# Kernel tuning notes

Measured on AMD Instinct MI355X. Metric: run time of the kernel, lower is better.

Reference implementation:

```python
import jax, jax.numpy as jnp
import numpy as np

IN_DIM = 300
MEM_DIM = 1024
DEPTH = 14  # perfect binary tree in heap order: N = 2**DEPTH - 1 = 16383 nodes


def _init_linear(key, out_dim, in_dim):
    # torch nn.Linear default init: U(-1/sqrt(in), 1/sqrt(in)) for W and b
    s = 1.0 / np.sqrt(in_dim)
    kw, kb = jax.random.split(key)
    W = jax.random.uniform(kw, (out_dim, in_dim), jnp.float32, -s, s)
    b = jax.random.uniform(kb, (out_dim,), jnp.float32, -s, s)
    return W, b


def setup_inputs() -> dict:
    key = jax.random.key(0)
    keys = jax.random.split(key, 9)
    N = 2 ** DEPTH - 1
    inp = {"embs": jax.random.normal(keys[0], (N, IN_DIM), jnp.float32)}
    gates = [("ix", IN_DIM), ("ih", MEM_DIM), ("fx", IN_DIM), ("fh", MEM_DIM),
             ("ox", IN_DIM), ("oh", MEM_DIM), ("ux", IN_DIM), ("uh", MEM_DIM)]
    for k, (name, d) in zip(keys[1:], gates):
        W, b = _init_linear(k, MEM_DIM, d)
        inp["W" + name] = W
        inp["b" + name] = b
    inp["depth"] = DEPTH
    return inp


def _lin(x, W, b):
    return x @ W.T + b


def reference(embs, Wix, bix, Wih, bih, Wfx, bfx, Wfh, bfh,
              Wox, box, Woh, boh, Wux, bux, Wuh, buh, depth):
    # Child-Sum TreeLSTM on a perfect binary tree (heap order), processed
    # bottom-up, batching all nodes of a level into single GEMMs.
    h = c = None
    for lvl in range(depth - 1, -1, -1):
        n = 2 ** lvl
        x = embs[n - 1:2 * n - 1]  # [n, in_dim], nodes of this level
        if h is None:
            # leaves: original code feeds a single zero child -> h_sum = 0
            # and f * child_c = 0 regardless of f
            hsum = jnp.zeros((n, MEM_DIM), embs.dtype)
            fc = jnp.zeros((n, MEM_DIM), embs.dtype)
        else:
            hc = h.reshape(n, 2, MEM_DIM)  # children hidden states
            cc = c.reshape(n, 2, MEM_DIM)  # children cell states
            hsum = hc.sum(axis=1)
            # per-child forget gate: sigmoid(fh(h_k) + fx(x))
            f = jax.nn.sigmoid(jnp.einsum('nkd,md->nkm', hc, Wfh) + bfh
                               + _lin(x, Wfx, bfx)[:, None, :])
            fc = (f * cc).sum(axis=1)
        i = jax.nn.sigmoid(_lin(x, Wix, bix) + _lin(hsum, Wih, bih))
        o = jax.nn.sigmoid(_lin(x, Wox, box) + _lin(hsum, Woh, boh))
        u = jnp.tanh(_lin(x, Wux, bux) + _lin(hsum, Wuh, buh))
        c = i * u + fc
        h = o * jnp.tanh(c)
    return jnp.stack([c[0], h[0]])  # root state (c, h): [2, MEM_DIM]
```

## Files before the change

### kernel.cpp

```cpp
#include <hip/hip_runtime.h>
#include <hip/hip_bf16.h>

#define IN_DIM 300
#define XDIM   320
#define MEM    1024
#define NTREE  16383

typedef _Float16 half8 __attribute__((ext_vector_type(8)));
typedef float    f32x4 __attribute__((ext_vector_type(4)));

__device__ __forceinline__ float sigf(float x) { return 1.0f / (1.0f + __expf(-x)); }
__device__ __forceinline__ float tanhfast(float x) { return 2.0f / (1.0f + __expf(-2.0f * x)) - 1.0f; }

#define GLOAD_LDS16(g, l) \
    __builtin_amdgcn_global_load_lds((const __attribute__((address_space(1))) void*)(g), \
                                     (__attribute__((address_space(3))) void*)(l), 16, 0, 0)

__global__ void pack_kernel(
    const float* __restrict__ embs,
    const float* __restrict__ Wix, const float* __restrict__ bix,
    const float* __restrict__ Wih, const float* __restrict__ bih,
    const float* __restrict__ Wfx, const float* __restrict__ bfx,
    const float* __restrict__ Wfh, const float* __restrict__ bfh,
    const float* __restrict__ Wox, const float* __restrict__ box_,
    const float* __restrict__ Woh, const float* __restrict__ boh,
    const float* __restrict__ Wux, const float* __restrict__ bux,
    const float* __restrict__ Wuh, const float* __restrict__ buh,
    _Float16* __restrict__ Wiou16, _Float16* __restrict__ Wfh16,
    _Float16* __restrict__ x16, _Float16* __restrict__ Bx)
{
    long long idx = (long long)blockIdx.x * blockDim.x + threadIdx.x;
    const long long n_wiou = 3072LL * 1024;
    const long long n_wfh  = 1024LL * 1024;
    const long long n_x    = 16384LL * XDIM;
    const long long n_bx   = 4096LL * XDIM;
    if (idx < n_wiou) {
        int m = (int)(idx >> 10), k = (int)(idx & 1023);
        int g = m >> 10, mm = m & 1023;
        const float* W = (g == 0) ? Wih : (g == 1) ? Woh : Wuh;
        Wiou16[idx] = (_Float16)W[(long long)mm * MEM + k];
        return;
    }
    idx -= n_wiou;
    if (idx < n_wfh) {
        Wfh16[idx] = (_Float16)Wfh[idx];
        return;
    }
    idx -= n_wfh;
    if (idx < n_x) {
        int node = (int)(idx / XDIM), j = (int)(idx % XDIM);
        float v = 0.f;
        if (node < NTREE) {
            if (j < IN_DIM) v = embs[(long long)node * IN_DIM + j];
            else if (j == IN_DIM) v = 1.0f;
        }
        x16[idx] = (_Float16)v;
        return;
    }
    idx -= n_x;
    if (idx < n_bx) {
        int r = (int)(idx / XDIM), j = (int)(idx % XDIM);
        int g = r >> 10, mm = r & 1023;
        const float* Wx = (g == 0) ? Wix : (g == 1) ? Wox : (g == 2) ? Wux : Wfx;
        const float* b1 = (g == 0) ? bix : (g == 1) ? box_ : (g == 2) ? bux : bfx;
        const float* b2 = (g == 0) ? bih : (g == 1) ? boh : (g == 2) ? buh : bfh;
        float v = 0.f;
        if (j < IN_DIM) v = Wx[(long long)mm * IN_DIM + j];
        else if (j == IN_DIM) v = b1[mm] + b2[mm];
        Bx[idx] = (_Float16)v;
    }
}

template<int BM, int BN, int BK>
__device__ __forceinline__ void gemm_tile(
    const _Float16* __restrict__ A, int lda,
    const _Float16* __restrict__ B, int ldb,
    _Float16* __restrict__ C, int ldc, int K,
    _Float16* ldsA, _Float16* ldsB)
{
    constexpr int FM = BM / 32, FN = BN / 32;
    constexpr int CPR = BK / 8;
    constexpr int SWM = CPR - 1;
    constexpr int ACH = BM * BK / 2048;
    constexpr int BCH = BN * BK / 2048;

    int tid = threadIdx.x, wave = tid >> 6, lane = tid & 63;
    int wr = (wave >> 1) * (BM / 2), wc = (wave & 1) * (BN / 2);
    int kq = (lane >> 4) * 8, rs = lane & 15;
    f32x4 acc[FM][FN] = {};

    for (int k0 = 0; k0 < K; k0 += BK) {
#pragma unroll
        for (int j = 0; j < ACH; ++j) {
            int c = j * 256 + tid;
            int row = c / CPR;
            int s = (c ^ row) & SWM;
            GLOAD_LDS16(A + (long long)row * lda + k0 + s * 8,
                        &ldsA[(j * 256 + wave * 64) * 8]);
        }
#pragma unroll
        for (int j = 0; j < BCH; ++j) {
            int c = j * 256 + tid;
            int row = c / CPR;
            int s = (c ^ row) & SWM;
            GLOAD_LDS16(B + (long long)row * ldb + k0 + s * 8,
                        &ldsB[(j * 256 + wave * 64) * 8]);
        }
        __syncthreads();
#pragma unroll
        for (int kk = 0; kk < BK; kk += 32) {
            half8 a[FM], b[FN];
#pragma unroll
            for (int i = 0; i < FM; ++i) {
                int r = wr + i * 16 + rs;
                int s = ((kk + kq) >> 3) ^ (r & SWM);
                a[i] = *(const half8*)&ldsA[r * BK + s * 8];
            }
#pragma unroll
            for (int i = 0; i < FN; ++i) {
                int r = wc + i * 16 + rs;
                int s = ((kk + kq) >> 3) ^ (r & SWM);
                b[i] = *(const half8*)&ldsB[r * BK + s * 8];
            }
#pragma unroll
            for (int mi = 0; mi < FM; ++mi)
#pragma unroll
                for (int ni = 0; ni < FN; ++ni)
                    acc[mi][ni] = __builtin_amdgcn_mfma_f32_16x16x32_f16(a[mi], b[ni], acc[mi][ni], 0, 0, 0);
        }
        __syncthreads();
    }
    int crb = wr + (lane >> 4) * 4, ccb = wc + rs;
#pragma unroll
    for (int mi = 0; mi < FM; ++mi)
#pragma unroll
        for (int i = 0; i < 4; ++i) {
            long long r = crb + mi * 16 + i;
#pragma unroll
            for (int ni = 0; ni < FN; ++ni)
                C[r * ldc + ccb + ni * 16] = (_Float16)acc[mi][ni][i];
        }
}

template<int BM, int BN, int BK>
__global__ __launch_bounds__(256) void gemm_f16(
    const _Float16* __restrict__ A, int lda,
    const _Float16* __restrict__ B, int ldb,
    _Float16* __restrict__ C, int ldc, int K)
{
    __shared__ __align__(16) _Float16 ldsA[BM * BK];
    __shared__ __align__(16) _Float16 ldsB[BN * BK];
    gemm_tile<BM, BN, BK>(A + (long long)blockIdx.x * BM * lda, lda,
                          B + (long long)blockIdx.y * BN * ldb, ldb,
                          C + (long long)blockIdx.x * BM * ldc + (long long)blockIdx.y * BN,
                          ldc, K, ldsA, ldsB);
}

template<int BM1, int BM2, int BK>
__global__ __launch_bounds__(256) void gemm_level(
    const _Float16* __restrict__ Hsum, const _Float16* __restrict__ Hc,
    const _Float16* __restrict__ Wiou, const _Float16* __restrict__ Wf,
    _Float16* __restrict__ houpre, _Float16* __restrict__ fpre,
    int G1, int G2)
{
    constexpr int BMX = (BM1 > BM2) ? BM1 : BM2;
    __shared__ __align__(16) _Float16 ldsA[BMX * BK];
    __shared__ __align__(16) _Float16 ldsB[128 * BK];
    int bx = blockIdx.x;
    if (bx < G1 * 24) {
        int nb = bx / G1, mb = bx % G1;
        gemm_tile<BM1, 128, BK>(Hsum + (long long)mb * BM1 * 1024, 1024,
                                Wiou + (long long)nb * 128 * 1024, 1024,
                                houpre + (long long)mb * BM1 * 3072 + nb * 128, 3072,
                                1024, ldsA, ldsB);
    } else {
        int b2 = bx - G1 * 24;
        int nb = b2 / G2, mb = b2 % G2;
        gemm_tile<BM2, 128, BK>(Hc + (long long)mb * BM2 * 1024, 1024,
                                Wf + (long long)nb * 128 * 1024, 1024,
                                fpre + (long long)mb * BM2 * 1024 + nb * 128, 1024,
                                1024, ldsA, ldsB);
    }
}

__global__ void leaf_combine(const _Float16* __restrict__ XpI,
                             _Float16* __restrict__ cleaf,
                             _Float16* __restrict__ hout,
                             _Float16* __restrict__ hsum)
{
    int idx = blockIdx.x * blockDim.x + threadIdx.x;
    int r = idx >> 7, m8 = (idx & 127) * 8;
    float hs[8];
#pragma unroll
    for (int j = 0; j < 8; ++j) hs[j] = 0.f;
#pragma unroll
    for (int t = 0; t < 2; ++t) {
        long long l = 2 * r + t;
        long long node = 8191 + l;
        half8 vi = *(const half8*)&XpI[node * 3072 + m8];
        half8 vo = *(const half8*)&XpI[node * 3072 + 1024 + m8];
        half8 vu = *(const half8*)&XpI[node * 3072 + 2048 + m8];
        half8 cv, hv;
#pragma unroll
        for (int j = 0; j < 8; ++j) {
            float i = sigf((float)vi[j]);
            float o = sigf((float)vo[j]);
            float u = tanhfast((float)vu[j]);
            float c = i * u;
            float h = o * tanhfast(c);
            cv[j] = (_Float16)c; hv[j] = (_Float16)h; hs[j] += h;
        }
        *(half8*)&cleaf[l * 1024 + m8] = cv;
        *(half8*)&hout[l * 1024 + m8] = hv;
    }
    half8 sv;
#pragma unroll
    for (int j = 0; j < 8; ++j) sv[j] = (_Float16)hs[j];
    *(half8*)&hsum[(long long)r * 1024 + m8] = sv;
}

template<bool C16>
__global__ void combine_level(
    const _Float16* __restrict__ houpre, const _Float16* __restrict__ fpre,
    const void* __restrict__ cprevp,
    const _Float16* __restrict__ XpI, const _Float16* __restrict__ XpF,
    float* __restrict__ cout, _Float16* __restrict__ hout, _Float16* __restrict__ hsum,
    int n, int gx0, float* __restrict__ fin)
{
    int idx = blockIdx.x * blockDim.x + threadIdx.x;
    int npairs = (n > 1) ? (n >> 1) : 1;
    if (idx >= npairs * 128) return;
    int r = idx >> 7, m8 = (idx & 127) * 8;
    float hs[8];
#pragma unroll
    for (int j = 0; j < 8; ++j) hs[j] = 0.f;
    int pmax = (n > 1) ? 2 : 1;
    for (int t = 0; t < pmax; ++t) {
        int p = 2 * r + t;
        long long node = gx0 + p;
        half8 phi = *(const half8*)&houpre[(long long)p * 3072 + m8];
        half8 pho = *(const half8*)&houpre[(long long)p * 3072 + 1024 + m8];
        half8 phu = *(const half8*)&houpre[(long long)p * 3072 + 2048 + m8];
        half8 pxi = *(const half8*)&XpI[node * 3072 + m8];
        half8 pxo = *(const half8*)&XpI[node * 3072 + 1024 + m8];
        half8 pxu = *(const half8*)&XpI[node * 3072 + 2048 + m8];
        half8 pf0 = *(const half8*)&fpre[(long long)(2 * p) * 1024 + m8];
        half8 pf1 = *(const half8*)&fpre[(long long)(2 * p + 1) * 1024 + m8];
        half8 pxf = *(const half8*)&XpF[node * 1024 + m8];
        float c0[8], c1[8];
        if (C16) {
            const _Float16* cp = (const _Float16*)cprevp;
            half8 a = *(const half8*)&cp[(long long)(2 * p) * 1024 + m8];
            half8 b = *(const half8*)&cp[(long long)(2 * p + 1) * 1024 + m8];
#pragma unroll
            for (int j = 0; j < 8; ++j) { c0[j] = (float)a[j]; c1[j] = (float)b[j]; }
        } else {
            const float* cp = (const float*)cprevp;
            f32x4 a0 = *(const f32x4*)&cp[(long long)(2 * p) * 1024 + m8];
            f32x4 a1 = *(const f32x4*)&cp[(long long)(2 * p) * 1024 + m8 + 4];
            f32x4 b0 = *(const f32x4*)&cp[(long long)(2 * p + 1) * 1024 + m8];
            f32x4 b1 = *(const f32x4*)&cp[(long long)(2 * p + 1) * 1024 + m8 + 4];
#pragma unroll
            for (int j = 0; j < 4; ++j) { c0[j] = a0[j]; c0[j + 4] = a1[j]; c1[j] = b0[j]; c1[j + 4] = b1[j]; }
        }
        float cw[8], hw[8];
#pragma unroll
        for (int j = 0; j < 8; ++j) {
            float i  = sigf((float)phi[j] + (float)pxi[j]);
            float o  = sigf((float)pho[j] + (float)pxo[j]);
            float u  = tanhfast((float)phu[j] + (float)pxu[j]);
            float f0 = sigf((float)pf0[j] + (float)pxf[j]);
            float f1 = sigf((float)pf1[j] + (float)pxf[j]);
            float c = i * u + f0 * c0[j] + f1 * c1[j];
            float h = o * tanhfast(c);
            cw[j] = c; hw[j] = h; hs[j] += h;
        }
        if (fin) {
            f32x4 v0 = {cw[0], cw[1], cw[2], cw[3]}, v1 = {cw[4], cw[5], cw[6], cw[7]};
            f32x4 w0 = {hw[0], hw[1], hw[2], hw[3]}, w1 = {hw[4], hw[5], hw[6], hw[7]};
            *(f32x4*)&fin[m8] = v0;            *(f32x4*)&fin[m8 + 4] = v1;
            *(f32x4*)&fin[1024 + m8] = w0;     *(f32x4*)&fin[1024 + m8 + 4] = w1;
        } else {
            f32x4 v0 = {cw[0], cw[1], cw[2], cw[3]}, v1 = {cw[4], cw[5], cw[6], cw[7]};
            *(f32x4*)&cout[(long long)p * 1024 + m8] = v0;
            *(f32x4*)&cout[(long long)p * 1024 + m8 + 4] = v1;
            half8 hv;
#pragma unroll
            for (int j = 0; j < 8; ++j) hv[j] = (_Float16)hw[j];
            *(half8*)&hout[(long long)p * 1024 + m8] = hv;
        }
    }
    if (!fin) {
        half8 sv;
#pragma unroll
        for (int j = 0; j < 8; ++j) sv[j] = (_Float16)hs[j];
        *(half8*)&hsum[(long long)r * 1024 + m8] = sv;
    }
}

extern "C" void kernel_launch(void* const* d_in, const int* in_sizes, int n_in,
                              void* d_out, int out_size, void* d_ws, size_t ws_size,
                              hipStream_t stream)
{
    const float* embs = (const float*)d_in[0];
    const float* Wix = (const float*)d_in[1];  const float* bix = (const float*)d_in[2];
    const float* Wih = (const float*)d_in[3];  const float* bih = (const float*)d_in[4];
    const float* Wfx = (const float*)d_in[5];  const float* bfx = (const float*)d_in[6];
    const float* Wfh = (const float*)d_in[7];  const float* bfh = (const float*)d_in[8];
    const float* Wox = (const float*)d_in[9];  const float* box_ = (const float*)d_in[10];
    const float* Woh = (const float*)d_in[11]; const float* boh = (const float*)d_in[12];
    const float* Wux = (const float*)d_in[13]; const float* bux = (const float*)d_in[14];
    const float* Wuh = (const float*)d_in[15]; const float* buh = (const float*)d_in[16];

    char* p = (char*)d_ws;
    auto carve = [&](size_t bytes) -> char* {
        char* r = p; p += (bytes + 255) & ~(size_t)255; return r;
    };
    _Float16* Wiou16 = (_Float16*)carve((size_t)3072 * 1024 * 2);
    _Float16* Wfh16  = (_Float16*)carve((size_t)1024 * 1024 * 2);
    _Float16* XpI    = (_Float16*)carve((size_t)16384 * 3072 * 2);
    _Float16* XpF    = (_Float16*)carve((size_t)8192 * 1024 * 2);
    _Float16* fpre   = (_Float16*)carve((size_t)8192 * 1024 * 2);
    _Float16* H_A    = (_Float16*)carve((size_t)8192 * 1024 * 2);
    _Float16* H_B    = (_Float16*)carve((size_t)4096 * 1024 * 2);
    _Float16* Hsum   = (_Float16*)carve((size_t)4096 * 1024 * 2);
    _Float16* Cleaf  = (_Float16*)carve((size_t)8192 * 1024 * 2);
    float*    Cping  = (float*)carve((size_t)4096 * 1024 * 4);
    float*    Cpong  = (float*)carve((size_t)2048 * 1024 * 4);
    _Float16* houpre = XpI + (size_t)8192 * 3072;
    _Float16* x16    = fpre;
    _Float16* Bx     = fpre + (size_t)16384 * XDIM;

    {
        long long tot = 3072LL * 1024 + 1024LL * 1024 + 16384LL * XDIM + 4096LL * XDIM;
        pack_kernel<<<dim3((int)((tot + 255) / 256)), dim3(256), 0, stream>>>(
            embs, Wix, bix, Wih, bih, Wfx, bfx, Wfh, bfh,
            Wox, box_, Woh, boh, Wux, bux, Wuh, buh,
            Wiou16, Wfh16, x16, Bx);
    }

    gemm_f16<128, 128, 32><<<dim3(128, 24), dim3(256), 0, stream>>>(
        x16, XDIM, Bx, XDIM, XpI, 3072, XDIM);
    gemm_f16<128, 128, 32><<<dim3(64, 8), dim3(256), 0, stream>>>(
        x16, XDIM, Bx + (size_t)3072 * XDIM, XDIM, XpF, 1024, XDIM);

    leaf_combine<<<dim3(2048), dim3(256), 0, stream>>>(XpI, Cleaf, H_A, Hsum);

    const void* cprev = Cleaf;
    float* cbufs[2] = {Cping, Cpong};
    int ci = 0;
    _Float16* hcur = H_A;
    _Float16* hnext = H_B;

    for (int lvl = 12; lvl >= 0; --lvl) {
        int n = 1 << lvl;
        int G1, G2;
        if (n >= 1024) {
            G1 = n / 128; G2 = 2 * n / 128;
            gemm_level<128, 128, 32><<<dim3(G1 * 24 + G2 * 8), dim3(256), 0, stream>>>(
                Hsum, hcur, Wiou16, Wfh16, houpre, fpre, G1, G2);
        } else if (n >= 128) {
            G1 = n / 128; G2 = 2 * n / 128;
            gemm_level<128, 128, 128><<<dim3(G1 * 24 + G2 * 8), dim3(256), 0, stream>>>(
                Hsum, hcur, Wiou16, Wfh16, houpre, fpre, G1, G2);
        } else if (n == 64) {
            G1 = 1; G2 = 1;
            gemm_level<64, 128, 128><<<dim3(G1 * 24 + G2 * 8), dim3(256), 0, stream>>>(
                Hsum, hcur, Wiou16, Wfh16, houpre, fpre, G1, G2);
        } else {
            G1 = 1; G2 = 1;
            gemm_level<64, 64, 128><<<dim3(G1 * 24 + G2 * 8), dim3(256), 0, stream>>>(
                Hsum, hcur, Wiou16, Wfh16, houpre, fpre, G1, G2);
        }

        int npairs = (n > 1) ? (n >> 1) : 1;
        int blocks = (npairs * 128 + 255) / 256;
        float* fin = (lvl == 0) ? (float*)d_out : nullptr;
        if (lvl == 12)
            combine_level<true><<<dim3(blocks), dim3(256), 0, stream>>>(
                houpre, fpre, cprev, XpI, XpF, cbufs[ci], hnext, Hsum, n, n - 1, fin);
        else
            combine_level<false><<<dim3(blocks), dim3(256), 0, stream>>>(
                houpre, fpre, cprev, XpI, XpF, cbufs[ci], hnext, Hsum, n, n - 1, fin);

        cprev = cbufs[ci];
        ci ^= 1;
        _Float16* tmp = hcur; hcur = hnext; hnext = tmp;
    }
}
```

Measured before the change: 461.2 us.

## Fuse leaf GEMM with combine, fuse small levels, double-buffer GEMM tiles

The leaf input projection and the leaf gate math are merged into one kernel, so the leaf half of the XpI pre-activations is never written to or read back from memory. Levels below 512 nodes now run a single fused kernel that does both GEMMs plus the cell update, which removes a launch and a round-trip through houpre/fpre for each of those levels. The shared GEMM tile gains LDS double buffering, and BK is raised to 64 for the large GEMMs. The cost is higher LDS use and register pressure, and the fused small-level kernels use narrow 64×64 tiles with many accumulators.

New measurement: 662.2 us. 1.44x slower.

```diff
diff --git a/kernel.cpp b/kernel.cpp
--- a/kernel.cpp
+++ b/kernel.cpp
@@ -79,24 +79,22 @@
     _Float16* ldsA, _Float16* ldsB)
 {
     constexpr int FM = BM / 32, FN = BN / 32;
-    constexpr int CPR = BK / 8;
-    constexpr int SWM = CPR - 1;
-    constexpr int ACH = BM * BK / 2048;
-    constexpr int BCH = BN * BK / 2048;
+    constexpr int CPR = BK / 8, SWM = CPR - 1;
+    constexpr int ACH = BM * BK / 2048, BCH = BN * BK / 2048;
 
     int tid = threadIdx.x, wave = tid >> 6, lane = tid & 63;
     int wr = (wave >> 1) * (BM / 2), wc = (wave & 1) * (BN / 2);
     int kq = (lane >> 4) * 8, rs = lane & 15;
     f32x4 acc[FM][FN] = {};
 
-    for (int k0 = 0; k0 < K; k0 += BK) {
+    auto stage = [&](int buf, int k0) {
 #pragma unroll
         for (int j = 0; j < ACH; ++j) {
             int c = j * 256 + tid;
             int row = c / CPR;
             int s = (c ^ row) & SWM;
             GLOAD_LDS16(A + (long long)row * lda + k0 + s * 8,
-                        &ldsA[(j * 256 + wave * 64) * 8]);
+                        &ldsA[buf * BM * BK + (j * 256 + wave * 64) * 8]);
         }
 #pragma unroll
         for (int j = 0; j < BCH; ++j) {
@@ -104,9 +102,17 @@
             int row = c / CPR;
             int s = (c ^ row) & SWM;
             GLOAD_LDS16(B + (long long)row * ldb + k0 + s * 8,
-                        &ldsB[(j * 256 + wave * 64) * 8]);
-        }
-        __syncthreads();
+                        &ldsB[buf * BN * BK + (j * 256 + wave * 64) * 8]);
+        }
+    };
+
+    int NT = K / BK;
+    stage(0, 0);
+    __syncthreads();
+    for (int t = 0; t < NT; ++t) {
+        if (t + 1 < NT) stage((t + 1) & 1, (t + 1) * BK);
+        const _Float16* bA = ldsA + (t & 1) * BM * BK;
+        const _Float16* bB = ldsB + (t & 1) * BN * BK;
 #pragma unroll
         for (int kk = 0; kk < BK; kk += 32) {
             half8 a[FM], b[FN];
@@ -114,13 +120,13 @@
             for (int i = 0; i < FM; ++i) {
                 int r = wr + i * 16 + rs;
                 int s = ((kk + kq) >> 3) ^ (r & SWM);
-                a[i] = *(const half8*)&ldsA[r * BK + s * 8];
+                a[i] = *(const half8*)&bA[r * BK + s * 8];
             }
 #pragma unroll
             for (int i = 0; i < FN; ++i) {
                 int r = wc + i * 16 + rs;
                 int s = ((kk + kq) >> 3) ^ (r & SWM);
-                b[i] = *(const half8*)&ldsB[r * BK + s * 8];
+                b[i] = *(const half8*)&bB[r * BK + s * 8];
             }
 #pragma unroll
             for (int mi = 0; mi < FM; ++mi)
@@ -148,75 +154,232 @@
     const _Float16* __restrict__ B, int ldb,
     _Float16* __restrict__ C, int ldc, int K)
 {
-    __shared__ __align__(16) _Float16 ldsA[BM * BK];
-    __shared__ __align__(16) _Float16 ldsB[BN * BK];
+    __shared__ __align__(16) _Float16 ldsA[2 * BM * BK];
+    __shared__ __align__(16) _Float16 ldsB[2 * BN * BK];
     gemm_tile<BM, BN, BK>(A + (long long)blockIdx.x * BM * lda, lda,
                           B + (long long)blockIdx.y * BN * ldb, ldb,
                           C + (long long)blockIdx.x * BM * ldc + (long long)blockIdx.y * BN,
                           ldc, K, ldsA, ldsB);
 }
 
-template<int BM1, int BM2, int BK>
 __global__ __launch_bounds__(256) void gemm_level(
     const _Float16* __restrict__ Hsum, const _Float16* __restrict__ Hc,
     const _Float16* __restrict__ Wiou, const _Float16* __restrict__ Wf,
     _Float16* __restrict__ houpre, _Float16* __restrict__ fpre,
     int G1, int G2)
 {
-    constexpr int BMX = (BM1 > BM2) ? BM1 : BM2;
-    __shared__ __align__(16) _Float16 ldsA[BMX * BK];
-    __shared__ __align__(16) _Float16 ldsB[128 * BK];
+    __shared__ __align__(16) _Float16 ldsA[2 * 128 * 64];
+    __shared__ __align__(16) _Float16 ldsB[2 * 128 * 64];
     int bx = blockIdx.x;
     if (bx < G1 * 24) {
         int nb = bx / G1, mb = bx % G1;
-        gemm_tile<BM1, 128, BK>(Hsum + (long long)mb * BM1 * 1024, 1024,
+        gemm_tile<128, 128, 64>(Hsum + (long long)mb * 128 * 1024, 1024,
                                 Wiou + (long long)nb * 128 * 1024, 1024,
-                                houpre + (long long)mb * BM1 * 3072 + nb * 128, 3072,
+                                houpre + (long long)mb * 128 * 3072 + nb * 128, 3072,
                                 1024, ldsA, ldsB);
     } else {
         int b2 = bx - G1 * 24;
         int nb = b2 / G2, mb = b2 % G2;
-        gemm_tile<BM2, 128, BK>(Hc + (long long)mb * BM2 * 1024, 1024,
+        gemm_tile<128, 128, 64>(Hc + (long long)mb * 128 * 1024, 1024,
                                 Wf + (long long)nb * 128 * 1024, 1024,
-                                fpre + (long long)mb * BM2 * 1024 + nb * 128, 1024,
+                                fpre + (long long)mb * 128 * 1024 + nb * 128, 1024,
                                 1024, ldsA, ldsB);
     }
 }
 
-__global__ void leaf_combine(const _Float16* __restrict__ XpI,
-                             _Float16* __restrict__ cleaf,
-                             _Float16* __restrict__ hout,
-                             _Float16* __restrict__ hsum)
-{
-    int idx = blockIdx.x * blockDim.x + threadIdx.x;
-    int r = idx >> 7, m8 = (idx & 127) * 8;
-    float hs[8];
-#pragma unroll
-    for (int j = 0; j < 8; ++j) hs[j] = 0.f;
-#pragma unroll
-    for (int t = 0; t < 2; ++t) {
-        long long l = 2 * r + t;
-        long long node = 8191 + l;
-        half8 vi = *(const half8*)&XpI[node * 3072 + m8];
-        half8 vo = *(const half8*)&XpI[node * 3072 + 1024 + m8];
-        half8 vu = *(const half8*)&XpI[node * 3072 + 2048 + m8];
-        half8 cv, hv;
-#pragma unroll
-        for (int j = 0; j < 8; ++j) {
-            float i = sigf((float)vi[j]);
-            float o = sigf((float)vo[j]);
-            float u = tanhfast((float)vu[j]);
-            float c = i * u;
-            float h = o * tanhfast(c);
-            cv[j] = (_Float16)c; hv[j] = (_Float16)h; hs[j] += h;
-        }
-        *(half8*)&cleaf[l * 1024 + m8] = cv;
-        *(half8*)&hout[l * 1024 + m8] = hv;
-    }
-    half8 sv;
-#pragma unroll
-    for (int j = 0; j < 8; ++j) sv[j] = (_Float16)hs[j];
-    *(half8*)&hsum[(long long)r * 1024 + m8] = sv;
+__global__ __launch_bounds__(256) void leaf_fused(
+    const _Float16* __restrict__ x16, const _Float16* __restrict__ Bx,
+    _Float16* __restrict__ cleaf, _Float16* __restrict__ hleaf,
+    _Float16* __restrict__ hsum)
+{
+    constexpr int BK = 32, CPR = 4, SWM = 3;
+    __shared__ __align__(16) _Float16 lA[2 * 64 * BK];
+    __shared__ __align__(16) _Float16 lB[2 * 384 * BK];
+    int tid = threadIdx.x, wave = tid >> 6, lane = tid & 63;
+    int kq = (lane >> 4) * 8, rs = lane & 15;
+    int wr = (wave >> 1) * 32, wc = (wave & 1) * 64;
+    int m0 = blockIdx.x * 64, c0 = blockIdx.y * 128;
+    const _Float16* A = x16 + (size_t)(8191 + m0) * XDIM;
+
+    auto stage = [&](int buf, int k0) {
+        {
+            int c = tid, row = c / CPR, s = (c ^ row) & SWM;
+            GLOAD_LDS16(A + (long long)row * XDIM + k0 + s * 8,
+                        &lA[buf * 64 * BK + (wave * 64) * 8]);
+        }
+#pragma unroll
+        for (int j = 0; j < 6; ++j) {
+            int c = j * 256 + tid;
+            int row = c / CPR, s = (c ^ row) & SWM;
+            int g = row >> 7, rr = row & 127;
+            GLOAD_LDS16(Bx + (long long)(g * 1024 + c0 + rr) * XDIM + k0 + s * 8,
+                        &lB[buf * 384 * BK + (j * 256 + wave * 64) * 8]);
+        }
+    };
+    f32x4 acc[3][2][4] = {};
+    stage(0, 0);
+    __syncthreads();
+    for (int t = 0; t < 10; ++t) {
+        if (t + 1 < 10) stage((t + 1) & 1, (t + 1) * BK);
+        const _Float16* bA = lA + (t & 1) * 64 * BK;
+        const _Float16* bB = lB + (t & 1) * 384 * BK;
+        half8 a[2], b[3][4];
+#pragma unroll
+        for (int mi = 0; mi < 2; ++mi) {
+            int r = wr + mi * 16 + rs;
+            int s = (kq >> 3) ^ (r & SWM);
+            a[mi] = *(const half8*)&bA[r * BK + s * 8];
+        }
+#pragma unroll
+        for (int g = 0; g < 3; ++g)
+#pragma unroll
+            for (int nj = 0; nj < 4; ++nj) {
+                int r = g * 128 + wc + nj * 16 + rs;
+                int s = (kq >> 3) ^ (r & SWM);
+                b[g][nj] = *(const half8*)&bB[r * BK + s * 8];
+            }
+#pragma unroll
+        for (int g = 0; g < 3; ++g)
+#pragma unroll
+            for (int mi = 0; mi < 2; ++mi)
+#pragma unroll
+                for (int nj = 0; nj < 4; ++nj)
+                    acc[g][mi][nj] = __builtin_amdgcn_mfma_f32_16x16x32_f16(a[mi], b[g][nj], acc[g][mi][nj], 0, 0, 0);
+        __syncthreads();
+    }
+    int lrb = wr + (lane >> 4) * 4;
+#pragma unroll
+    for (int mi = 0; mi < 2; ++mi)
+#pragma unroll
+        for (int nj = 0; nj < 4; ++nj) {
+            int col = c0 + wc + nj * 16 + rs;
+            float hpair = 0.f;
+#pragma unroll
+            for (int i = 0; i < 4; ++i) {
+                long long l = m0 + lrb + mi * 16 + i;
+                float cc = sigf(acc[0][mi][nj][i]) * 0.f +
+                           0.f;
+                float ip = acc[0][mi][nj][i];
+                float op = acc[1][mi][nj][i];
+                float up = acc[2][mi][nj][i];
+                cc = sigf(ip) * tanhfast(up);
+                float hh = sigf(op) * tanhfast(cc);
+                cleaf[l * 1024 + col] = (_Float16)cc;
+                hleaf[l * 1024 + col] = (_Float16)hh;
+                if (i & 1) hsum[(l >> 1) * 1024 + col] = (_Float16)(hpair + hh);
+                else hpair = hh;
+            }
+        }
+}
+
+__global__ __launch_bounds__(256) void level_fused(
+    const _Float16* __restrict__ Hs, const _Float16* __restrict__ Hc,
+    const _Float16* __restrict__ Wiou, const _Float16* __restrict__ Wf,
+    const float* __restrict__ cprev,
+    const _Float16* __restrict__ XpI, const _Float16* __restrict__ XpF,
+    float* __restrict__ cout, _Float16* __restrict__ hout,
+    _Float16* __restrict__ hsumout, int n, int gx0, float* __restrict__ fin)
+{
+    constexpr int BK = 32, CPR = 4, SWM = 3;
+    __shared__ __align__(16) _Float16 lA[2 * 192 * BK];
+    __shared__ __align__(16) _Float16 lB[2 * 256 * BK];
+    int tid = threadIdx.x, wave = tid >> 6, lane = tid & 63;
+    int kq = (lane >> 4) * 8, rs = lane & 15;
+    int wr = (wave >> 1) * 32, wc = (wave & 1) * 32;
+    int p0 = blockIdx.x * 64, c0 = blockIdx.y * 64;
+
+    auto stage = [&](int buf, int k0) {
+#pragma unroll
+        for (int j = 0; j < 3; ++j) {
+            int c = j * 256 + tid;
+            int row = c / CPR, s = (c ^ row) & SWM;
+            int ta = row >> 6, rr = row & 63;
+            const _Float16* src = (ta == 0) ? Hs : Hc;
+            long long grow = (ta == 0) ? (long long)(p0 + rr)
+                                       : (2LL * (p0 + rr) + (ta - 1));
+            GLOAD_LDS16(src + grow * 1024 + k0 + s * 8,
+                        &lA[buf * 192 * BK + (j * 256 + wave * 64) * 8]);
+        }
+#pragma unroll
+        for (int j = 0; j < 4; ++j) {
+            int c = j * 256 + tid;
+            int row = c / CPR, s = (c ^ row) & SWM;
+            int tb = row >> 6, rr = row & 63;
+            const _Float16* src = (tb < 3) ? Wiou : Wf;
+            long long grow = (tb < 3) ? (long long)(tb * 1024 + c0 + rr)
+                                      : (long long)(c0 + rr);
+            GLOAD_LDS16(src + grow * 1024 + k0 + s * 8,
+                        &lB[buf * 256 * BK + (j * 256 + wave * 64) * 8]);
+        }
+    };
+    f32x4 acc[5][2][2] = {};
+    stage(0, 0);
+    __syncthreads();
+    for (int t = 0; t < 32; ++t) {
+        if (t + 1 < 32) stage((t + 1) & 1, (t + 1) * BK);
+        const _Float16* bA = lA + (t & 1) * 192 * BK;
+        const _Float16* bB = lB + (t & 1) * 256 * BK;
+        half8 a[3][2], b[4][2];
+#pragma unroll
+        for (int ta = 0; ta < 3; ++ta)
+#pragma unroll
+            for (int mi = 0; mi < 2; ++mi) {
+                int r = ta * 64 + wr + mi * 16 + rs;
+                int s = (kq >> 3) ^ (r & SWM);
+                a[ta][mi] = *(const half8*)&bA[r * BK + s * 8];
+            }
+#pragma unroll
+        for (int tb = 0; tb < 4; ++tb)
+#pragma unroll
+            for (int nj = 0; nj < 2; ++nj) {
+                int r = tb * 64 + wc + nj * 16 + rs;
+                int s = (kq >> 3) ^ (r & SWM);
+                b[tb][nj] = *(const half8*)&bB[r * BK + s * 8];
+            }
+#pragma unroll
+        for (int mi = 0; mi < 2; ++mi)
+#pragma unroll
+            for (int nj = 0; nj < 2; ++nj) {
+                acc[0][mi][nj] = __builtin_amdgcn_mfma_f32_16x16x32_f16(a[0][mi], b[0][nj], acc[0][mi][nj], 0, 0, 0);
+                acc[1][mi][nj] = __builtin_amdgcn_mfma_f32_16x16x32_f16(a[0][mi], b[1][nj], acc[1][mi][nj], 0, 0, 0);
+                acc[2][mi][nj] = __builtin_amdgcn_mfma_f32_16x16x32_f16(a[0][mi], b[2][nj], acc[2][mi][nj], 0, 0, 0);
+                acc[3][mi][nj] = __builtin_amdgcn_mfma_f32_16x16x32_f16(a[1][mi], b[3][nj], acc[3][mi][nj], 0, 0, 0);
+                acc[4][mi][nj] = __builtin_amdgcn_mfma_f32_16x16x32_f16(a[2][mi], b[3][nj], acc[4][mi][nj], 0, 0, 0);
+            }
+        __syncthreads();
+    }
+    int lrb = wr + (lane >> 4) * 4;
+#pragma unroll
+    for (int mi = 0; mi < 2; ++mi)
+#pragma unroll
+        for (int nj = 0; nj < 2; ++nj) {
+            int col = c0 + wc + nj * 16 + rs;
+            float hpair = 0.f;
+#pragma unroll
+            for (int i = 0; i < 4; ++i) {
+                int p = p0 + lrb + mi * 16 + i;
+                if (p >= n) continue;
+                long long node = gx0 + p;
+                float ip = acc[0][mi][nj][i] + (float)XpI[node * 3072 + col];
+                float op = acc[1][mi][nj][i] + (float)XpI[node * 3072 + 1024 + col];
+                float up = acc[2][mi][nj][i] + (float)XpI[node * 3072 + 2048 + col];
+                float xf = (float)XpF[node * 1024 + col];
+                float f0 = sigf(acc[3][mi][nj][i] + xf);
+                float f1 = sigf(acc[4][mi][nj][i] + xf);
+                float cc = sigf(ip) * tanhfast(up)
+                         + f0 * cprev[(long long)(2 * p) * 1024 + col]
+                         + f1 * cprev[(long long)(2 * p + 1) * 1024 + col];
+                float hh = sigf(op) * tanhfast(cc);
+                if (fin) {
+                    if (p == 0) { fin[col] = cc; fin[1024 + col] = hh; }
+                } else {
+                    cout[(long long)p * 1024 + col] = cc;
+                    hout[(long long)p * 1024 + col] = (_Float16)hh;
+                    if (i & 1) hsumout[((long long)(p >> 1)) * 1024 + col] = (_Float16)(hpair + hh);
+                    else hpair = hh;
+                }
+            }
+        }
 }
 
 template<bool C16>
@@ -225,17 +388,16 @@
     const void* __restrict__ cprevp,
     const _Float16* __restrict__ XpI, const _Float16* __restrict__ XpF,
     float* __restrict__ cout, _Float16* __restrict__ hout, _Float16* __restrict__ hsum,
-    int n, int gx0, float* __restrict__ fin)
+    int n, int gx0)
 {
     int idx = blockIdx.x * blockDim.x + threadIdx.x;
-    int npairs = (n > 1) ? (n >> 1) : 1;
+    int npairs = n >> 1;
     if (idx >= npairs * 128) return;
     int r = idx >> 7, m8 = (idx & 127) * 8;
     float hs[8];
 #pragma unroll
     for (int j = 0; j < 8; ++j) hs[j] = 0.f;
-    int pmax = (n > 1) ? 2 : 1;
-    for (int t = 0; t < pmax; ++t) {
+    for (int t = 0; t < 2; ++t) {
         int p = 2 * r + t;
         long long node = gx0 + p;
         half8 phi = *(const half8*)&houpre[(long long)p * 3072 + m8];
@@ -275,27 +437,18 @@
             float h = o * tanhfast(c);
             cw[j] = c; hw[j] = h; hs[j] += h;
         }
-        if (fin) {
-            f32x4 v0 = {cw[0], cw[1], cw[2], cw[3]}, v1 = {cw[4], cw[5], cw[6], cw[7]};
-            f32x4 w0 = {hw[0], hw[1], hw[2], hw[3]}, w1 = {hw[4], hw[5], hw[6], hw[7]};
-            *(f32x4*)&fin[m8] = v0;            *(f32x4*)&fin[m8 + 4] = v1;
-            *(f32x4*)&fin[1024 + m8] = w0;     *(f32x4*)&fin[1024 + m8 + 4] = w1;
-        } else {
-            f32x4 v0 = {cw[0], cw[1], cw[2], cw[3]}, v1 = {cw[4], cw[5], cw[6], cw[7]};
-            *(f32x4*)&cout[(long long)p * 1024 + m8] = v0;
-            *(f32x4*)&cout[(long long)p * 1024 + m8 + 4] = v1;
-            half8 hv;
-#pragma unroll
-            for (int j = 0; j < 8; ++j) hv[j] = (_Float16)hw[j];
-            *(half8*)&hout[(long long)p * 1024 + m8] = hv;
-        }
-    }
-    if (!fin) {
-        half8 sv;
-#pragma unroll
-        for (int j = 0; j < 8; ++j) sv[j] = (_Float16)hs[j];
-        *(half8*)&hsum[(long long)r * 1024 + m8] = sv;
-    }
+        f32x4 v0 = {cw[0], cw[1], cw[2], cw[3]}, v1 = {cw[4], cw[5], cw[6], cw[7]};
+        *(f32x4*)&cout[(long long)p * 1024 + m8] = v0;
+        *(f32x4*)&cout[(long long)p * 1024 + m8 + 4] = v1;
+        half8 hv;
+#pragma unroll
+        for (int j = 0; j < 8; ++j) hv[j] = (_Float16)hw[j];
+        *(half8*)&hout[(long long)p * 1024 + m8] = hv;
+    }
+    half8 sv;
+#pragma unroll
+    for (int j = 0; j < 8; ++j) sv[j] = (_Float16)hs[j];
+    *(half8*)&hsum[(long long)r * 1024 + m8] = sv;
 }
 
 extern "C" void kernel_launch(void* const* d_in, const int* in_sizes, int n_in,
@@ -318,18 +471,19 @@
     };
     _Float16* Wiou16 = (_Float16*)carve((size_t)3072 * 1024 * 2);
     _Float16* Wfh16  = (_Float16*)carve((size_t)1024 * 1024 * 2);
-    _Float16* XpI    = (_Float16*)carve((size_t)16384 * 3072 * 2);
+    _Float16* XpI    = (_Float16*)carve((size_t)8192 * 3072 * 2);
     _Float16* XpF    = (_Float16*)carve((size_t)8192 * 1024 * 2);
+    _Float16* houpre = (_Float16*)carve((size_t)4096 * 3072 * 2);
     _Float16* fpre   = (_Float16*)carve((size_t)8192 * 1024 * 2);
     _Float16* H_A    = (_Float16*)carve((size_t)8192 * 1024 * 2);
     _Float16* H_B    = (_Float16*)carve((size_t)4096 * 1024 * 2);
-    _Float16* Hsum   = (_Float16*)carve((size_t)4096 * 1024 * 2);
+    _Float16* HsumA  = (_Float16*)carve((size_t)4096 * 1024 * 2);
+    _Float16* HsumB  = (_Float16*)carve((size_t)4096 * 1024 * 2);
     _Float16* Cleaf  = (_Float16*)carve((size_t)8192 * 1024 * 2);
     float*    Cping  = (float*)carve((size_t)4096 * 1024 * 4);
     float*    Cpong  = (float*)carve((size_t)2048 * 1024 * 4);
-    _Float16* houpre = XpI + (size_t)8192 * 3072;
-    _Float16* x16    = fpre;
-    _Float16* Bx     = fpre + (size_t)16384 * XDIM;
+    _Float16* x16 = fpre;
+    _Float16* Bx  = fpre + (size_t)16384 * XDIM;
 
     {
         long long tot = 3072LL * 1024 + 1024LL * 1024 + 16384LL * XDIM + 4096LL * XDIM;
@@ -339,52 +493,40 @@
             Wiou16, Wfh16, x16, Bx);
     }
 
-    gemm_f16<128, 128, 32><<<dim3(128, 24), dim3(256), 0, stream>>>(
+    gemm_f16<128, 128, 64><<<dim3(64, 24), dim3(256), 0, stream>>>(
         x16, XDIM, Bx, XDIM, XpI, 3072, XDIM);
-    gemm_f16<128, 128, 32><<<dim3(64, 8), dim3(256), 0, stream>>>(
+    gemm_f16<128, 128, 64><<<dim3(64, 8), dim3(256), 0, stream>>>(
         x16, XDIM, Bx + (size_t)3072 * XDIM, XDIM, XpF, 1024, XDIM);
-
-    leaf_combine<<<dim3(2048), dim3(256), 0, stream>>>(XpI, Cleaf, H_A, Hsum);
+    leaf_fused<<<dim3(128, 8), dim3(256), 0, stream>>>(x16, Bx, Cleaf, H_A, HsumA);
 
     const void* cprev = Cleaf;
     float* cbufs[2] = {Cping, Cpong};
-    int ci = 0;
+    _Float16* hsums[2] = {HsumA, HsumB};
+    int ci = 0, si = 0;
     _Float16* hcur = H_A;
     _Float16* hnext = H_B;
 
     for (int lvl = 12; lvl >= 0; --lvl) {
         int n = 1 << lvl;
-        int G1, G2;
-        if (n >= 1024) {
-            G1 = n / 128; G2 = 2 * n / 128;
-            gemm_level<128, 128, 32><<<dim3(G1 * 24 + G2 * 8), dim3(256), 0, stream>>>(
-                Hsum, hcur, Wiou16, Wfh16, houpre, fpre, G1, G2);
-        } else if (n >= 128) {
-            G1 = n / 128; G2 = 2 * n / 128;
-            gemm_level<128, 128, 128><<<dim3(G1 * 24 + G2 * 8), dim3(256), 0, stream>>>(
-                Hsum, hcur, Wiou16, Wfh16, houpre, fpre, G1, G2);
-        } else if (n == 64) {
-            G1 = 1; G2 = 1;
-            gemm_level<64, 128, 128><<<dim3(G1 * 24 + G2 * 8), dim3(256), 0, stream>>>(
-                Hsum, hcur, Wiou16, Wfh16, houpre, fpre, G1, G2);
+        float* fin = (lvl == 0) ? (float*)d_out : nullptr;
+        if (n >= 512) {
+            int G1 = n / 128, G2 = 2 * n / 128;
+            gemm_level<<<dim3(G1 * 24 + G2 * 8), dim3(256), 0, stream>>>(
+                hsums[si], hcur, Wiou16, Wfh16, houpre, fpre, G1, G2);
+            int blocks = ((n >> 1) * 128 + 255) / 256;
+            if (lvl == 12)
+                combine_level<true><<<dim3(blocks), dim3(256), 0, stream>>>(
+                    houpre, fpre, cprev, XpI, XpF, cbufs[ci], hnext, hsums[si ^ 1], n, n - 1);
+            else
+                combine_level<false><<<dim3(blocks), dim3(256), 0, stream>>>(
+                    houpre, fpre, cprev, XpI, XpF, cbufs[ci], hnext, hsums[si ^ 1], n, n - 1);
         } else {
-            G1 = 1; G2 = 1;
-            gemm_level<64, 64, 128><<<dim3(G1 * 24 + G2 * 8), dim3(256), 0, stream>>>(
-                Hsum, hcur, Wiou16, Wfh16, houpre, fpre, G1, G2);
-        }
-
-        int npairs = (n > 1) ? (n >> 1) : 1;
-        int blocks = (npairs * 128 + 255) / 256;
-        float* fin = (lvl == 0) ? (float*)d_out : nullptr;
-        if (lvl == 12)
-            combine_level<true><<<dim3(blocks), dim3(256), 0, stream>>>(
-                houpre, fpre, cprev, XpI, XpF, cbufs[ci], hnext, Hsum, n, n - 1, fin);
-        else
-            combine_level<false><<<dim3(blocks), dim3(256), 0, stream>>>(
-                houpre, fpre, cprev, XpI, XpF, cbufs[ci], hnext, Hsum, n, n - 1, fin);
-
+            level_fused<<<dim3((n + 63) / 64, 16), dim3(256), 0, stream>>>(
+                hsums[si], hcur, Wiou16, Wfh16, (const float*)cprev, XpI, XpF,
+                cbufs[ci], hnext, hsums[si ^ 1], n, n - 1, fin);
+        }
         cprev = cbufs[ci];
-        ci ^= 1;
+        ci ^= 1; si ^= 1;
         _Float16* tmp = hcur; hcur = hnext; hnext = tmp;
     }
 }
```

## Fuse leaf x-projection GEMM with leaf combine and merge internal x-projections

Applied to the files above, without the earlier changes.

Leaf nodes no longer get their x-projections written to memory. A new fused kernel computes the i/o/u projections for leaves with MFMA and applies the gate nonlinearities directly in registers, writing c, h and pairwise h sums. Internal nodes now use a single GEMM that produces a combined 4096-wide i/o/u/f projection buffer, replacing two separate GEMMs. Hsum is double-buffered because combine writes the next level's sum while the current one is being read. This saves the leaf projection's write and read-back and one launch, at the cost of scattered scalar fp16 stores in the leaf epilogue.

New measurement: 448.8 us (median of 2 runs). 2.7% less time.

```diff
diff --git a/kernel.cpp b/kernel.cpp
--- a/kernel.cpp
+++ b/kernel.cpp
@@ -79,10 +79,8 @@
     _Float16* ldsA, _Float16* ldsB)
 {
     constexpr int FM = BM / 32, FN = BN / 32;
-    constexpr int CPR = BK / 8;
-    constexpr int SWM = CPR - 1;
-    constexpr int ACH = BM * BK / 2048;
-    constexpr int BCH = BN * BK / 2048;
+    constexpr int CPR = BK / 8, SWM = CPR - 1;
+    constexpr int ACH = BM * BK / 2048, BCH = BN * BK / 2048;
 
     int tid = threadIdx.x, wave = tid >> 6, lane = tid & 63;
     int wr = (wave >> 1) * (BM / 2), wc = (wave & 1) * (BN / 2);
@@ -183,47 +181,85 @@
     }
 }
 
-__global__ void leaf_combine(const _Float16* __restrict__ XpI,
-                             _Float16* __restrict__ cleaf,
-                             _Float16* __restrict__ hout,
-                             _Float16* __restrict__ hsum)
-{
-    int idx = blockIdx.x * blockDim.x + threadIdx.x;
-    int r = idx >> 7, m8 = (idx & 127) * 8;
-    float hs[8];
-#pragma unroll
-    for (int j = 0; j < 8; ++j) hs[j] = 0.f;
-#pragma unroll
-    for (int t = 0; t < 2; ++t) {
-        long long l = 2 * r + t;
-        long long node = 8191 + l;
-        half8 vi = *(const half8*)&XpI[node * 3072 + m8];
-        half8 vo = *(const half8*)&XpI[node * 3072 + 1024 + m8];
-        half8 vu = *(const half8*)&XpI[node * 3072 + 2048 + m8];
-        half8 cv, hv;
-#pragma unroll
-        for (int j = 0; j < 8; ++j) {
-            float i = sigf((float)vi[j]);
-            float o = sigf((float)vo[j]);
-            float u = tanhfast((float)vu[j]);
-            float c = i * u;
-            float h = o * tanhfast(c);
-            cv[j] = (_Float16)c; hv[j] = (_Float16)h; hs[j] += h;
-        }
-        *(half8*)&cleaf[l * 1024 + m8] = cv;
-        *(half8*)&hout[l * 1024 + m8] = hv;
-    }
-    half8 sv;
-#pragma unroll
-    for (int j = 0; j < 8; ++j) sv[j] = (_Float16)hs[j];
-    *(half8*)&hsum[(long long)r * 1024 + m8] = sv;
+__global__ __launch_bounds__(256) void leaf_fused(
+    const _Float16* __restrict__ x16, const _Float16* __restrict__ Bx,
+    _Float16* __restrict__ cleaf, _Float16* __restrict__ hleaf,
+    _Float16* __restrict__ hsum)
+{
+    constexpr int BK = 32, CPR = 4, SWM = 3;
+    __shared__ __align__(16) _Float16 lA[64 * BK];
+    __shared__ __align__(16) _Float16 lB[384 * BK];
+    int tid = threadIdx.x, wave = tid >> 6, lane = tid & 63;
+    int kq = (lane >> 4) * 8, rs = lane & 15;
+    int wr = (wave >> 1) * 32, wc = (wave & 1) * 64;
+    int m0 = blockIdx.x * 64, c0 = blockIdx.y * 128;
+    const _Float16* A = x16 + (size_t)(8191 + m0) * XDIM;
+
+    f32x4 acc[3][2][4] = {};
+    for (int t = 0; t < 10; ++t) {
+        int k0 = t * BK;
+        {
+            int c = tid, row = c / CPR, s = (c ^ row) & SWM;
+            GLOAD_LDS16(A + (long long)row * XDIM + k0 + s * 8, &lA[(wave * 64) * 8]);
+        }
+#pragma unroll
+        for (int j = 0; j < 6; ++j) {
+            int c = j * 256 + tid;
+            int row = c / CPR, s = (c ^ row) & SWM;
+            int g = row >> 7, rr = row & 127;
+            GLOAD_LDS16(Bx + (long long)(g * 1024 + c0 + rr) * XDIM + k0 + s * 8,
+                        &lB[(j * 256 + wave * 64) * 8]);
+        }
+        __syncthreads();
+        half8 a[2], b[3][4];
+#pragma unroll
+        for (int mi = 0; mi < 2; ++mi) {
+            int r = wr + mi * 16 + rs;
+            int s = (kq >> 3) ^ (r & SWM);
+            a[mi] = *(const half8*)&lA[r * BK + s * 8];
+        }
+#pragma unroll
+        for (int g = 0; g < 3; ++g)
+#pragma unroll
+            for (int nj = 0; nj < 4; ++nj) {
+                int r = g * 128 + wc + nj * 16 + rs;
+                int s = (kq >> 3) ^ (r & SWM);
+                b[g][nj] = *(const half8*)&lB[r * BK + s * 8];
+            }
+#pragma unroll
+        for (int g = 0; g < 3; ++g)
+#pragma unroll
+            for (int mi = 0; mi < 2; ++mi)
+#pragma unroll
+                for (int nj = 0; nj < 4; ++nj)
+                    acc[g][mi][nj] = __builtin_amdgcn_mfma_f32_16x16x32_f16(a[mi], b[g][nj], acc[g][mi][nj], 0, 0, 0);
+        __syncthreads();
+    }
+    int lrb = wr + (lane >> 4) * 4;
+#pragma unroll
+    for (int mi = 0; mi < 2; ++mi)
+#pragma unroll
+        for (int nj = 0; nj < 4; ++nj) {
+            int col = c0 + wc + nj * 16 + rs;
+            float hpair = 0.f;
+#pragma unroll
+            for (int i = 0; i < 4; ++i) {
+                long long l = m0 + lrb + mi * 16 + i;
+                float cc = sigf(acc[0][mi][nj][i]) * tanhfast(acc[2][mi][nj][i]);
+                float hh = sigf(acc[1][mi][nj][i]) * tanhfast(cc);
+                cleaf[l * 1024 + col] = (_Float16)cc;
+                hleaf[l * 1024 + col] = (_Float16)hh;
+                if (i & 1) hsum[(l >> 1) * 1024 + col] = (_Float16)(hpair + hh);
+                else hpair = hh;
+            }
+        }
 }
 
 template<bool C16>
 __global__ void combine_level(
     const _Float16* __restrict__ houpre, const _Float16* __restrict__ fpre,
     const void* __restrict__ cprevp,
-    const _Float16* __restrict__ XpI, const _Float16* __restrict__ XpF,
+    const _Float16* __restrict__ Xp,
     float* __restrict__ cout, _Float16* __restrict__ hout, _Float16* __restrict__ hsum,
     int n, int gx0, float* __restrict__ fin)
 {
@@ -241,12 +277,12 @@
         half8 phi = *(const half8*)&houpre[(long long)p * 3072 + m8];
         half8 pho = *(const half8*)&houpre[(long long)p * 3072 + 1024 + m8];
         half8 phu = *(const half8*)&houpre[(long long)p * 3072 + 2048 + m8];
-        half8 pxi = *(const half8*)&XpI[node * 3072 + m8];
-        half8 pxo = *(const half8*)&XpI[node * 3072 + 1024 + m8];
-        half8 pxu = *(const half8*)&XpI[node * 3072 + 2048 + m8];
+        half8 pxi = *(const half8*)&Xp[node * 4096 + m8];
+        half8 pxo = *(const half8*)&Xp[node * 4096 + 1024 + m8];
+        half8 pxu = *(const half8*)&Xp[node * 4096 + 2048 + m8];
+        half8 pxf = *(const half8*)&Xp[node * 4096 + 3072 + m8];
         half8 pf0 = *(const half8*)&fpre[(long long)(2 * p) * 1024 + m8];
         half8 pf1 = *(const half8*)&fpre[(long long)(2 * p + 1) * 1024 + m8];
-        half8 pxf = *(const half8*)&XpF[node * 1024 + m8];
         float c0[8], c1[8];
         if (C16) {
             const _Float16* cp = (const _Float16*)cprevp;
@@ -318,18 +354,18 @@
     };
     _Float16* Wiou16 = (_Float16*)carve((size_t)3072 * 1024 * 2);
     _Float16* Wfh16  = (_Float16*)carve((size_t)1024 * 1024 * 2);
-    _Float16* XpI    = (_Float16*)carve((size_t)16384 * 3072 * 2);
-    _Float16* XpF    = (_Float16*)carve((size_t)8192 * 1024 * 2);
+    _Float16* Xp     = (_Float16*)carve((size_t)8192 * 4096 * 2);
+    _Float16* houpre = (_Float16*)carve((size_t)4096 * 3072 * 2);
     _Float16* fpre   = (_Float16*)carve((size_t)8192 * 1024 * 2);
     _Float16* H_A    = (_Float16*)carve((size_t)8192 * 1024 * 2);
     _Float16* H_B    = (_Float16*)carve((size_t)4096 * 1024 * 2);
-    _Float16* Hsum   = (_Float16*)carve((size_t)4096 * 1024 * 2);
+    _Float16* HsumA  = (_Float16*)carve((size_t)4096 * 1024 * 2);
+    _Float16* HsumB  = (_Float16*)carve((size_t)4096 * 1024 * 2);
     _Float16* Cleaf  = (_Float16*)carve((size_t)8192 * 1024 * 2);
     float*    Cping  = (float*)carve((size_t)4096 * 1024 * 4);
     float*    Cpong  = (float*)carve((size_t)2048 * 1024 * 4);
-    _Float16* houpre = XpI + (size_t)8192 * 3072;
-    _Float16* x16    = fpre;
-    _Float16* Bx     = fpre + (size_t)16384 * XDIM;
+    _Float16* x16 = fpre;
+    _Float16* Bx  = fpre + (size_t)16384 * XDIM;
 
     {
         long long tot = 3072LL * 1024 + 1024LL * 1024 + 16384LL * XDIM + 4096LL * XDIM;
@@ -339,16 +375,14 @@
             Wiou16, Wfh16, x16, Bx);
     }
 
-    gemm_f16<128, 128, 32><<<dim3(128, 24), dim3(256), 0, stream>>>(
-        x16, XDIM, Bx, XDIM, XpI, 3072, XDIM);
-    gemm_f16<128, 128, 32><<<dim3(64, 8), dim3(256), 0, stream>>>(
-        x16, XDIM, Bx + (size_t)3072 * XDIM, XDIM, XpF, 1024, XDIM);
-
-    leaf_combine<<<dim3(2048), dim3(256), 0, stream>>>(XpI, Cleaf, H_A, Hsum);
+    gemm_f16<128, 128, 32><<<dim3(64, 32), dim3(256), 0, stream>>>(
+        x16, XDIM, Bx, XDIM, Xp, 4096, XDIM);
+    leaf_fused<<<dim3(128, 8), dim3(256), 0, stream>>>(x16, Bx, Cleaf, H_A, HsumA);
 
     const void* cprev = Cleaf;
     float* cbufs[2] = {Cping, Cpong};
-    int ci = 0;
+    _Float16* hsums[2] = {HsumA, HsumB};
+    int ci = 0, si = 0;
     _Float16* hcur = H_A;
     _Float16* hnext = H_B;
 
@@ -358,19 +392,19 @@
         if (n >= 1024) {
             G1 = n / 128; G2 = 2 * n / 128;
             gemm_level<128, 128, 32><<<dim3(G1 * 24 + G2 * 8), dim3(256), 0, stream>>>(
-                Hsum, hcur, Wiou16, Wfh16, houpre, fpre, G1, G2);
+                hsums[si], hcur, Wiou16, Wfh16, houpre, fpre, G1, G2);
         } else if (n >= 128) {
             G1 = n / 128; G2 = 2 * n / 128;
             gemm_level<128, 128, 128><<<dim3(G1 * 24 + G2 * 8), dim3(256), 0, stream>>>(
-                Hsum, hcur, Wiou16, Wfh16, houpre, fpre, G1, G2);
+                hsums[si], hcur, Wiou16, Wfh16, houpre, fpre, G1, G2);
         } else if (n == 64) {
             G1 = 1; G2 = 1;
             gemm_level<64, 128, 128><<<dim3(G1 * 24 + G2 * 8), dim3(256), 0, stream>>>(
-                Hsum, hcur, Wiou16, Wfh16, houpre, fpre, G1, G2);
+                hsums[si], hcur, Wiou16, Wfh16, houpre, fpre, G1, G2);
         } else {
             G1 = 1; G2 = 1;
             gemm_level<64, 64, 128><<<dim3(G1 * 24 + G2 * 8), dim3(256), 0, stream>>>(
-                Hsum, hcur, Wiou16, Wfh16, houpre, fpre, G1, G2);
+                hsums[si], hcur, Wiou16, Wfh16, houpre, fpre, G1, G2);
         }
 
         int npairs = (n > 1) ? (n >> 1) : 1;
@@ -378,13 +412,13 @@
         float* fin = (lvl == 0) ? (float*)d_out : nullptr;
         if (lvl == 12)
             combine_level<true><<<dim3(blocks), dim3(256), 0, stream>>>(
-                houpre, fpre, cprev, XpI, XpF, cbufs[ci], hnext, Hsum, n, n - 1, fin);
+                houpre, fpre, cprev, Xp, cbufs[ci], hnext, hsums[si ^ 1], n, n - 1, fin);
         else
             combine_level<false><<<dim3(blocks), dim3(256), 0, stream>>>(
-                houpre, fpre, cprev, XpI, XpF, cbufs[ci], hnext, Hsum, n, n - 1, fin);
+                houpre, fpre, cprev, Xp, cbufs[ci], hnext, hsums[si ^ 1], n, n - 1, fin);
 
         cprev = cbufs[ci];
-        ci ^= 1;
+        ci ^= 1; si ^= 1;
         _Float16* tmp = hcur; hcur = hnext; hnext = tmp;
     }
 }
```
